# Kernel optimization log

Hardware: AMD Instinct MI355X
Metric: run time of the kernel (lower is better)

## Reference

```python
import jax, jax.numpy as jnp
import numpy as np


def setup_inputs() -> dict:
    key = jax.random.key(0)
    ks = jax.random.split(key, 5)
    B, C_in, C_out, H, W, k = 16, 64, 64, 256, 256, 16
    scale = 1.0 / (C_in * C_out)
    return {
        "u": jax.random.normal(ks[0], (B, C_in, H, W), dtype=jnp.float32),
        "W_pos_re": scale * jax.random.normal(ks[1], (C_in, C_out, k, k), dtype=jnp.float32),
        "W_pos_im": scale * jax.random.normal(ks[2], (C_in, C_out, k, k), dtype=jnp.float32),
        "W_neg_re": scale * jax.random.normal(ks[3], (C_in, C_out, k, k), dtype=jnp.float32),
        "W_neg_im": scale * jax.random.normal(ks[4], (C_in, C_out, k, k), dtype=jnp.float32),
    }


def reference(u, W_pos_re, W_pos_im, W_neg_re, W_neg_im):
    B, C_in, H, W = u.shape
    C_out = W_pos_re.shape[1]
    k = W_pos_re.shape[2]
    W_half = W // 2 + 1
    k_h = min(k, H // 2)
    k_w = min(k, W_half)

    R_pos = (W_pos_re + 1j * W_pos_im)[:, :, :k_h, :k_w]  # (C_in, C_out, k_h, k_w)
    R_neg = (W_neg_re + 1j * W_neg_im)[:, :, :k_h, :k_w]

    u_hat = jnp.fft.rfft2(u, norm="ortho")  # (B, C_in, H, W_half) complex

    # spectral multiply on retained modes only
    top = jnp.einsum("bchw,cohw->bohw", u_hat[:, :, :k_h, :k_w], R_pos)
    bot = jnp.einsum("bchw,cohw->bohw", u_hat[:, :, H - k_h:, :k_w], R_neg)

    v_hat = jnp.zeros((B, C_out, H, W_half), dtype=u_hat.dtype)
    v_hat = v_hat.at[:, :, :k_h, :k_w].set(top)
    v_hat = v_hat.at[:, :, H - k_h:, :k_w].set(bot)

    return jnp.fft.irfft2(v_hat, s=(H, W), norm="ortho")  # (B, C_out, H, W) real
```

## Files before the change

kernel.cpp:

```cpp
#include <hip/hip_runtime.h>


#define B_    16
#define H_    256
#define W_    256

#define OFF_CT 0
#define OFF_ST 256
#define OFF_RP 512
#define RP_SZ  (512*4096*2)
#define OFF_U  (OFF_RP + RP_SZ)
#define U_SZ   (1024*512*2)
#define OFF_V  (OFF_U + U_SZ)

#define UTP   260
#define TWOPI_256 0.024543692606170259f

typedef const __attribute__((address_space(1))) void g_void;
typedef __attribute__((address_space(3))) void l_void;

__device__ __forceinline__ void load_lds16(const float* g, float* l) {
    __builtin_amdgcn_global_load_lds((g_void*)g, (l_void*)l, 16, 0, 0);
}

__global__ __launch_bounds__(256) void k_fwd1(const float* __restrict__ u,
                                              const float* __restrict__ wpr,
                                              const float* __restrict__ wpi,
                                              const float* __restrict__ wnr,
                                              const float* __restrict__ wni,
                                              float* __restrict__ ws,
                                              float* __restrict__ P) {
    __shared__ __align__(16) float ut[32][UTP];
    int t = threadIdx.x;

    if (blockIdx.x >= 8192) {
        int mw = blockIdx.x - 8192;
        int m = mw >> 4, wmc = mw & 15;
        const float* wr; const float* wi; int i;
        if (m < 16) { wr = wpr; wi = wpi; i = m; }
        else        { wr = wnr; wi = wni; i = m - 16; }
        if (mw == 0) {
            double a = 2.0 * 3.14159265358979323846 * (double)t / 256.0;
            ws[OFF_CT + t] = (float)cos(a);
            ws[OFF_ST + t] = (float)sin(a);
        }
        float norm = (wmc == 0 ? 1.f : 2.f) * (1.f / 65536.f);
        int off = i * 16 + wmc;
        float2* rp = (float2*)(ws + OFF_RP) + (size_t)mw * 4096;
        #pragma unroll
        for (int k = 0; k < 16; ++k) {
            int co = t + 256 * k;
            rp[co] = make_float2(wr[(size_t)co * 256 + off] * norm,
                                 wi[(size_t)co * 256 + off] * norm);
        }
        return;
    }

    int bc = blockIdx.x >> 3, ch = blockIdx.x & 7;
    const float* ub = u + (size_t)bc * 65536 + ch * 8192;
    int lane = t & 63, w = t >> 6;
    #pragma unroll
    for (int k = 0; k < 8; ++k)
        load_lds16(ub + (w * 8 + k) * 256 + lane * 4, &ut[w * 8 + k][0]);

    int h = lane & 7, r8 = lane >> 3;
    int rowc = w * 8 + r8;
    int wm0 = 2 * h, wm1 = wm0 + 1;
    float s0v, c0v, s1v, c1v;
    __sincosf(TWOPI_256 * (float)wm0, &s0v, &c0v);
    __sincosf(TWOPI_256 * (float)wm1, &s1v, &c1v);
    float r0r = c0v, r0i = -s0v;
    float r1r = c1v, r1i = -s1v;
    float bs  = (h & 1) ? -1.f : 1.f;
    float dsg = (h & 1) ? 1.f : -1.f;

    float p0r = 0.f, p0i = 0.f, p1r = 0.f, p1i = 0.f;
    float t0r = 1.f, t0i = 0.f, t1r = 1.f, t1i = 0.f;

    asm volatile("s_waitcnt vmcnt(0)" ::: "memory");

    const float* rowp = &ut[rowc][0];
    #pragma unroll 4
    for (int bat = 0; bat < 16; ++bat) {
        const float* rp = rowp + 4 * bat;
        float4 q0 = *(const float4*)(rp);
        float4 q1 = *(const float4*)(rp + 64);
        float4 q2 = *(const float4*)(rp + 128);
        float4 q3 = *(const float4*)(rp + 192);
        #define PROC_(u0, u1, u2, u3) {                                   \
            float a_ = (u0) + (u2), b_ = (u1) + (u3);                     \
            float c_ = (u0) - (u2), d_ = (u1) - (u3);                     \
            float g0 = fmaf(bs, b_, a_);                                  \
            float g1r = c_, g1i = dsg * d_;                               \
            p0r = fmaf(g0, t0r, p0r);                                     \
            p0i = fmaf(g0, t0i, p0i);                                     \
            p1r = fmaf(g1r, t1r, fmaf(-g1i, t1i, p1r));                   \
            p1i = fmaf(g1r, t1i, fmaf( g1i, t1r, p1i));                   \
            float n0r = t0r * r0r - t0i * r0i;                            \
            float n0i = t0r * r0i + t0i * r0r;                            \
            float n1r = t1r * r1r - t1i * r1i;                            \
            float n1i = t1r * r1i + t1i * r1r;                            \
            t0r = n0r; t0i = n0i; t1r = n1r; t1i = n1i; }
        PROC_(q0.x, q1.x, q2.x, q3.x)
        PROC_(q0.y, q1.y, q2.y, q3.y)
        PROC_(q0.z, q1.z, q2.z, q3.z)
        PROC_(q0.w, q1.w, q2.w, q3.w)
        #undef PROC_
    }
    int y = ch * 32 + rowc;
    ((float4*)P)[((size_t)bc * 256 + y) * 8 + h] = make_float4(p0r, p0i, p1r, p1i);
}

__global__ __launch_bounds__(256) void k_fwd2(const float* __restrict__ P,
                                              float* __restrict__ ws) {
    __shared__ float Pl[256][36];
    int t = threadIdx.x, bc = blockIdx.x;
    const float4* Pg = (const float4*)(P + (size_t)bc * 8192);
    #pragma unroll
    for (int k = 0; k < 8; ++k) {
        int f4 = t + 256 * k;
        int y = f4 >> 3, q = f4 & 7;
        *(float4*)&Pl[y][q * 4] = Pg[f4];
    }
    __syncthreads();

    int wm = t & 15;
    int v  = t >> 4;
    int m1 = ((v & 3) << 2) | (v >> 2);
    float sv, cv;
    __sincosf(TWOPI_256 * (float)m1, &sv, &cv);
    float r1r = cv, r1i = -sv;
    __sincosf(TWOPI_256 * (float)(m1 - 16), &sv, &cv);
    float r2r = cv, r2i = -sv;
    float t1r = 1.f, t1i = 0.f, t2r = 1.f, t2i = 0.f;
    float U1r = 0.f, U1i = 0.f, U2r = 0.f, U2i = 0.f;
    int md = m1 & 3;
    #pragma unroll 4
    for (int yy = 0; yy < 64; ++yy) {
        float2 P0 = *(float2*)&Pl[yy][2 * wm];
        float2 P1 = *(float2*)&Pl[yy + 64][2 * wm];
        float2 P2 = *(float2*)&Pl[yy + 128][2 * wm];
        float2 P3 = *(float2*)&Pl[yy + 192][2 * wm];
        float ar = P0.x + P2.x, ai = P0.y + P2.y;
        float br = P1.x + P3.x, bi = P1.y + P3.y;
        float cr = P0.x - P2.x, ci = P0.y - P2.y;
        float dr = P1.x - P3.x, di = P1.y - P3.y;
        float gr, gi;
        if (md == 0)      { gr = ar + br; gi = ai + bi; }
        else if (md == 1) { gr = cr + di; gi = ci - dr; }
        else if (md == 2) { gr = ar - br; gi = ai - bi; }
        else              { gr = cr - di; gi = ci + dr; }
        U1r = fmaf(gr, t1r, fmaf(-gi, t1i, U1r));
        U1i = fmaf(gr, t1i, fmaf( gi, t1r, U1i));
        U2r = fmaf(gr, t2r, fmaf(-gi, t2i, U2r));
        U2i = fmaf(gr, t2i, fmaf( gi, t2r, U2i));
        float n1r = t1r * r1r - t1i * r1i, n1i = t1r * r1i + t1i * r1r;
        float n2r = t2r * r2r - t2i * r2i, n2i = t2r * r2i + t2i * r2r;
        t1r = n1r; t1i = n1i; t2r = n2r; t2i = n2i;
    }
    float2* U = (float2*)(ws + OFF_U) + (size_t)bc * 512;
    U[m1 * 16 + wm]          = make_float2(U1r, U1i);
    U[(m1 + 16) * 16 + wm]   = make_float2(U2r, U2i);
}

__global__ __launch_bounds__(256) void k_cgemm(float* __restrict__ ws) {
    __shared__ float2 Ul[1024];
    int mw = blockIdx.x, t = threadIdx.x;
    const float2* Ug = (const float2*)(ws + OFF_U);
    #pragma unroll
    for (int k = 0; k < 4; ++k) {
        int bcv = t + 256 * k;
        Ul[bcv] = Ug[(size_t)bcv * 512 + mw];
    }
    __syncthreads();
    int o = t & 63, bq = t >> 6;
    const float2* rp = (const float2*)(ws + OFF_RP) + (size_t)mw * 4096;
    float ar[4] = {0.f, 0.f, 0.f, 0.f}, ai[4] = {0.f, 0.f, 0.f, 0.f};
    #pragma unroll 4
    for (int c = 0; c < 64; ++c) {
        float2 R = rp[c * 64 + o];
        #pragma unroll
        for (int j = 0; j < 4; ++j) {
            float2 Uv = Ul[(bq * 4 + j) * 64 + c];
            ar[j] = fmaf(Uv.x, R.x, fmaf(-Uv.y, R.y, ar[j]));
            ai[j] = fmaf(Uv.x, R.y, fmaf( Uv.y, R.x, ai[j]));
        }
    }
    float2* Vg = (float2*)(ws + OFF_V) + (size_t)mw * 1024;
    #pragma unroll
    for (int j = 0; j < 4; ++j)
        Vg[(bq * 4 + j) * 64 + o] = make_float2(ar[j], ai[j]);
}

__global__ __launch_bounds__(256) void k_inv(const float* __restrict__ ws,
                                             float* __restrict__ out) {
    __shared__ float Vl[16][68];
    __shared__ float Tl[4][16][36];
    __shared__ float ct[256], st[256];
    int t = threadIdx.x;
    int bo = blockIdx.x >> 2, q = blockIdx.x & 3;
    ct[t] = ws[OFF_CT + t];
    st[t] = ws[OFF_ST + t];
    {
        const float2* Vg = (const float2*)(ws + OFF_V);
        float2 v0 = Vg[(size_t)t * 1024 + bo];
        float2 v1 = Vg[(size_t)(t + 256) * 1024 + bo];
        int m = t >> 4, wmv = t & 15;
        Vl[wmv][2 * m]        = v0.x;  Vl[wmv][2 * m + 1]        = v0.y;
        Vl[wmv][2 * (m + 16)] = v1.x;  Vl[wmv][2 * (m + 16) + 1] = v1.y;
    }
    __syncthreads();

    int wm4 = t & 15, yb = t >> 4;
    int y0 = q * 16 + yb;
    float vr[32], vi[32];
    #pragma unroll
    for (int m = 0; m < 32; ++m) { vr[m] = Vl[wm4][2 * m]; vi[m] = Vl[wm4][2 * m + 1]; }
    float cy = ct[y0], sy = st[y0];
    float T0r=0,T0i=0,T1r=0,T1i=0,T2r=0,T2i=0,T3r=0,T3i=0;
    float tr = 1.f, ti = 0.f;
    #pragma unroll
    for (int m = 0; m < 32; ++m) {
        if (m == 16) {
            int i16 = (4096 - 16 * y0) & 255;
            tr = ct[i16]; ti = st[i16];
        }
        float hr = vr[m] * tr - vi[m] * ti;
        float hi = vr[m] * ti + vi[m] * tr;
        const int md = m & 3;
        T0r += hr; T0i += hi;
        if (md == 0)      { T1r += hr; T1i += hi; T2r += hr; T2i += hi; T3r += hr; T3i += hi; }
        else if (md == 1) { T1r -= hi; T1i += hr; T2r -= hr; T2i -= hi; T3r += hi; T3i -= hr; }
        else if (md == 2) { T1r -= hr; T1i -= hi; T2r += hr; T2i += hi; T3r -= hr; T3i -= hi; }
        else              { T1r += hi; T1i -= hr; T2r -= hr; T2i -= hi; T3r -= hi; T3i += hr; }
        float nr = tr * cy - ti * sy, ni = tr * sy + ti * cy;
        tr = nr; ti = ni;
    }
    Tl[0][yb][wm4] = T0r; Tl[0][yb][16 + wm4] = T0i;
    Tl[1][yb][wm4] = T1r; Tl[1][yb][16 + wm4] = T1i;
    Tl[2][yb][wm4] = T2r; Tl[2][yb][16 + wm4] = T2i;
    Tl[3][yb][wm4] = T3r; Tl[3][yb][16 + wm4] = T3i;
    __syncthreads();

    int l = t & 63, wv = t >> 6;
    float c0[16], s0[16];
    #pragma unroll
    for (int wm = 0; wm < 16; ++wm) {
        int idx = (wm * l) & 255;
        c0[wm] = ct[idx]; s0[wm] = st[idx];
    }
    float* ob = out + (size_t)bo * 65536;
    for (int yi = 0; yi < 16; ++yi) {
        int y = wv * 64 + q * 16 + yi;
        float TR[16], TI[16];
        const float4* rowv = (const float4*)&Tl[wv][yi][0];
        #pragma unroll
        for (int qq = 0; qq < 4; ++qq) {
            float4 a = rowv[qq];
            TR[4*qq]=a.x; TR[4*qq+1]=a.y; TR[4*qq+2]=a.z; TR[4*qq+3]=a.w;
            float4 b = rowv[qq + 4];
            TI[4*qq]=b.x; TI[4*qq+1]=b.y; TI[4*qq+2]=b.z; TI[4*qq+3]=b.w;
        }
        float Pv = 0.f, Qv = 0.f, Rv = 0.f, Sv = 0.f;
        #pragma unroll
        for (int wm = 0; wm < 16; wm += 2) {
            Pv = fmaf(TR[wm],     c0[wm],     Pv);
            Rv = fmaf(TI[wm],     s0[wm],     Rv);
            Qv = fmaf(TR[wm + 1], c0[wm + 1], Qv);
            Sv = fmaf(TI[wm + 1], s0[wm + 1], Sv);
        }
        float Ac = Pv + Qv, Bs = Rv + Sv;
        float Dc = Pv - Qv, Es = Rv - Sv;
        float* row = ob + (size_t)y * 256;
        row[l]               = Ac - Bs;
        row[(256 - l) & 255] = Ac + Bs;
        row[128 + l]         = Dc - Es;
        row[128 - l]         = Dc + Es;
        float E0 = TR[0] + TR[4] + TR[8]  + TR[12];
        float E2 = TR[2] + TR[6] + TR[10] + TR[14];
        float O1 = TI[1] + TI[5] + TI[9]  + TI[13];
        float O3 = TI[3] + TI[7] + TI[11] + TI[15];
        float EC = E0 - E2, OC = O1 - O3;
        if (l == 0) {
            row[64]  = EC - OC;
            row[192] = EC + OC;
        }
    }
}

extern "C" void kernel_launch(void* const* d_in, const int* in_sizes, int n_in,
                              void* d_out, int out_size, void* d_ws, size_t ws_size,
                              hipStream_t stream) {
    const float* u   = (const float*)d_in[0];
    const float* wpr = (const float*)d_in[1];
    const float* wpi = (const float*)d_in[2];
    const float* wnr = (const float*)d_in[3];
    const float* wni = (const float*)d_in[4];
    float* out = (float*)d_out;
    float* ws  = (float*)d_ws;
    float* P   = (float*)d_out;

    hipLaunchKernelGGL(k_fwd1,  dim3(8704), dim3(256), 0, stream, u, wpr, wpi, wnr, wni, ws, P);
    hipLaunchKernelGGL(k_fwd2,  dim3(1024), dim3(256), 0, stream, P, ws);
    hipLaunchKernelGGL(k_cgemm, dim3(512),  dim3(256), 0, stream, ws);
    hipLaunchKernelGGL(k_inv,   dim3(4096), dim3(256), 0, stream, ws, out);
}
```

Baseline: 207.1 us.

## Read input directly in fwd1 and split fwd2 column DFT across two blocks

```diff
diff --git a/kernel.cpp b/kernel.cpp
--- a/kernel.cpp
+++ b/kernel.cpp
@@ -9,19 +9,13 @@
 #define OFF_ST 256
 #define OFF_RP 512
 #define RP_SZ  (512*4096*2)
-#define OFF_U  (OFF_RP + RP_SZ)
+#define OFF_U0 (OFF_RP + RP_SZ)
 #define U_SZ   (1024*512*2)
-#define OFF_V  (OFF_U + U_SZ)
-
-#define UTP   260
+#define OFF_V  (OFF_U0 + U_SZ)
+#define V_SZ   (512*1024*2)
+#define OFF_U1 (OFF_V + V_SZ)
+
 #define TWOPI_256 0.024543692606170259f
-
-typedef const __attribute__((address_space(1))) void g_void;
-typedef __attribute__((address_space(3))) void l_void;
-
-__device__ __forceinline__ void load_lds16(const float* g, float* l) {
-    __builtin_amdgcn_global_load_lds((g_void*)g, (l_void*)l, 16, 0, 0);
-}
 
 __global__ __launch_bounds__(256) void k_fwd1(const float* __restrict__ u,
                                               const float* __restrict__ wpr,
@@ -30,7 +24,6 @@
                                               const float* __restrict__ wni,
                                               float* __restrict__ ws,
                                               float* __restrict__ P) {
-    __shared__ __align__(16) float ut[32][UTP];
     int t = threadIdx.x;
 
     if (blockIdx.x >= 8192) {
@@ -57,14 +50,11 @@
     }
 
     int bc = blockIdx.x >> 3, ch = blockIdx.x & 7;
-    const float* ub = u + (size_t)bc * 65536 + ch * 8192;
     int lane = t & 63, w = t >> 6;
-    #pragma unroll
-    for (int k = 0; k < 8; ++k)
-        load_lds16(ub + (w * 8 + k) * 256 + lane * 4, &ut[w * 8 + k][0]);
-
     int h = lane & 7, r8 = lane >> 3;
     int rowc = w * 8 + r8;
+    const float* rowp = u + (size_t)bc * 65536 + ch * 8192 + rowc * 256;
+
     int wm0 = 2 * h, wm1 = wm0 + 1;
     float s0v, c0v, s1v, c1v;
     __sincosf(TWOPI_256 * (float)wm0, &s0v, &c0v);
@@ -77,16 +67,13 @@
     float p0r = 0.f, p0i = 0.f, p1r = 0.f, p1i = 0.f;
     float t0r = 1.f, t0i = 0.f, t1r = 1.f, t1i = 0.f;
 
-    asm volatile("s_waitcnt vmcnt(0)" ::: "memory");
-
-    const float* rowp = &ut[rowc][0];
     #pragma unroll 4
     for (int bat = 0; bat < 16; ++bat) {
-        const float* rp = rowp + 4 * bat;
-        float4 q0 = *(const float4*)(rp);
-        float4 q1 = *(const float4*)(rp + 64);
-        float4 q2 = *(const float4*)(rp + 128);
-        float4 q3 = *(const float4*)(rp + 192);
+        const float4* rp4 = (const float4*)(rowp + 4 * bat);
+        float4 q0 = rp4[0];
+        float4 q1 = rp4[16];
+        float4 q2 = rp4[32];
+        float4 q3 = rp4[48];
         #define PROC_(u0, u1, u2, u3) {                                   \
             float a_ = (u0) + (u2), b_ = (u1) + (u3);                     \
             float c_ = (u0) - (u2), d_ = (u1) - (u3);                     \
@@ -113,14 +100,15 @@
 
 __global__ __launch_bounds__(256) void k_fwd2(const float* __restrict__ P,
                                               float* __restrict__ ws) {
-    __shared__ float Pl[256][36];
-    int t = threadIdx.x, bc = blockIdx.x;
+    __shared__ float Pl[4][32][36];
+    int t = threadIdx.x;
+    int bc = blockIdx.x >> 1, hh = blockIdx.x & 1;
     const float4* Pg = (const float4*)(P + (size_t)bc * 8192);
     #pragma unroll
-    for (int k = 0; k < 8; ++k) {
-        int f4 = t + 256 * k;
-        int y = f4 >> 3, q = f4 & 7;
-        *(float4*)&Pl[y][q * 4] = Pg[f4];
+    for (int k = 0; k < 4; ++k) {
+        int idx = t + 256 * k;
+        int g = idx >> 8, j = (idx >> 3) & 31, q = idx & 7;
+        *(float4*)&Pl[g][j][4 * q] = Pg[(size_t)(hh * 32 + j + 64 * g) * 8 + q];
     }
     __syncthreads();
 
@@ -132,15 +120,17 @@
     float r1r = cv, r1i = -sv;
     __sincosf(TWOPI_256 * (float)(m1 - 16), &sv, &cv);
     float r2r = cv, r2i = -sv;
-    float t1r = 1.f, t1i = 0.f, t2r = 1.f, t2i = 0.f;
+    int a0 = (m1 * 32 * hh) & 255;
+    __sincosf(TWOPI_256 * (float)a0, &sv, &cv);
+    float t1r = cv, t1i = -sv, t2r = cv, t2i = -sv;
     float U1r = 0.f, U1i = 0.f, U2r = 0.f, U2i = 0.f;
     int md = m1 & 3;
     #pragma unroll 4
-    for (int yy = 0; yy < 64; ++yy) {
-        float2 P0 = *(float2*)&Pl[yy][2 * wm];
-        float2 P1 = *(float2*)&Pl[yy + 64][2 * wm];
-        float2 P2 = *(float2*)&Pl[yy + 128][2 * wm];
-        float2 P3 = *(float2*)&Pl[yy + 192][2 * wm];
+    for (int j = 0; j < 32; ++j) {
+        float2 P0 = *(float2*)&Pl[0][j][2 * wm];
+        float2 P1 = *(float2*)&Pl[1][j][2 * wm];
+        float2 P2 = *(float2*)&Pl[2][j][2 * wm];
+        float2 P3 = *(float2*)&Pl[3][j][2 * wm];
         float ar = P0.x + P2.x, ai = P0.y + P2.y;
         float br = P1.x + P3.x, bi = P1.y + P3.y;
         float cr = P0.x - P2.x, ci = P0.y - P2.y;
@@ -158,19 +148,22 @@
         float n2r = t2r * r2r - t2i * r2i, n2i = t2r * r2i + t2i * r2r;
         t1r = n1r; t1i = n1i; t2r = n2r; t2i = n2i;
     }
-    float2* U = (float2*)(ws + OFF_U) + (size_t)bc * 512;
-    U[m1 * 16 + wm]          = make_float2(U1r, U1i);
-    U[(m1 + 16) * 16 + wm]   = make_float2(U2r, U2i);
+    float2* U = (float2*)(ws + (hh ? OFF_U1 : OFF_U0)) + (size_t)bc * 512;
+    U[m1 * 16 + wm]        = make_float2(U1r, U1i);
+    U[(m1 + 16) * 16 + wm] = make_float2(U2r, U2i);
 }
 
 __global__ __launch_bounds__(256) void k_cgemm(float* __restrict__ ws) {
     __shared__ float2 Ul[1024];
     int mw = blockIdx.x, t = threadIdx.x;
-    const float2* Ug = (const float2*)(ws + OFF_U);
+    const float2* Ug0 = (const float2*)(ws + OFF_U0);
+    const float2* Ug1 = (const float2*)(ws + OFF_U1);
     #pragma unroll
     for (int k = 0; k < 4; ++k) {
         int bcv = t + 256 * k;
-        Ul[bcv] = Ug[(size_t)bcv * 512 + mw];
+        float2 a = Ug0[(size_t)bcv * 512 + mw];
+        float2 b = Ug1[(size_t)bcv * 512 + mw];
+        Ul[bcv] = make_float2(a.x + b.x, a.y + b.y);
     }
     __syncthreads();
     int o = t & 63, bq = t >> 6;
@@ -301,7 +294,7 @@
     float* P   = (float*)d_out;
 
     hipLaunchKernelGGL(k_fwd1,  dim3(8704), dim3(256), 0, stream, u, wpr, wpi, wnr, wni, ws, P);
-    hipLaunchKernelGGL(k_fwd2,  dim3(1024), dim3(256), 0, stream, P, ws);
+    hipLaunchKernelGGL(k_fwd2,  dim3(2048), dim3(256), 0, stream, P, ws);
     hipLaunchKernelGGL(k_cgemm, dim3(512),  dim3(256), 0, stream, ws);
     hipLaunchKernelGGL(k_inv,   dim3(4096), dim3(256), 0, stream, ws, out);
 }
```

After: 233.1 us. 1.13x slower.

## Split row DFT across lane quads and reduce partial sums with DPP

Applied to the files above, without the earlier changes.

```diff
diff --git a/kernel.cpp b/kernel.cpp
--- a/kernel.cpp
+++ b/kernel.cpp
@@ -1,9 +1,5 @@
 #include <hip/hip_runtime.h>
 
-
-#define B_    16
-#define H_    256
-#define W_    256
 
 #define OFF_CT 0
 #define OFF_ST 256
@@ -21,6 +17,12 @@
 
 __device__ __forceinline__ void load_lds16(const float* g, float* l) {
     __builtin_amdgcn_global_load_lds((g_void*)g, (l_void*)l, 16, 0, 0);
+}
+
+template<int CTRL>
+__device__ __forceinline__ float dppf(float x) {
+    return __int_as_float(__builtin_amdgcn_update_dpp(
+        0, __float_as_int(x), CTRL, 0xF, 0xF, true));
 }
 
 __global__ __launch_bounds__(256) void k_fwd1(const float* __restrict__ u,
@@ -63,52 +65,85 @@
     for (int k = 0; k < 8; ++k)
         load_lds16(ub + (w * 8 + k) * 256 + lane * 4, &ut[w * 8 + k][0]);
 
-    int h = lane & 7, r8 = lane >> 3;
+    int s = lane & 3, h = (lane >> 2) & 1, r8 = lane >> 3;
     int rowc = w * 8 + r8;
-    int wm0 = 2 * h, wm1 = wm0 + 1;
-    float s0v, c0v, s1v, c1v;
-    __sincosf(TWOPI_256 * (float)wm0, &s0v, &c0v);
-    __sincosf(TWOPI_256 * (float)wm1, &s1v, &c1v);
-    float r0r = c0v, r0i = -s0v;
-    float r1r = c1v, r1i = -s1v;
-    float bs  = (h & 1) ? -1.f : 1.f;
-    float dsg = (h & 1) ? 1.f : -1.f;
-
-    float p0r = 0.f, p0i = 0.f, p1r = 0.f, p1i = 0.f;
-    float t0r = 1.f, t0i = 0.f, t1r = 1.f, t1i = 0.f;
+
+    float sv, cv;
+    __sincosf(TWOPI_256 * 1.f, &sv, &cv);
+    float rb1r = cv, rb1i = -sv;
+    __sincosf(TWOPI_256 * (float)(8 * h), &sv, &cv);
+    float r8hr = cv, r8hi = -sv;
+    int j0 = 16 * s;
+    __sincosf(TWOPI_256 * (float)((8 * h * j0) & 255), &sv, &cv);
+    float tw0r = cv, tw0i = -sv;
+    __sincosf(TWOPI_256 * (float)j0, &sv, &cv);
+    float bjr = cv, bji = -sv;
+
+    float a0r=0,a0i=0,a1r=0,a1i=0,a2r=0,a2i=0,a3r=0,a3i=0;
+    float a4r=0,a4i=0,a5r=0,a5i=0,a6r=0,a6i=0,a7r=0,a7i=0;
 
     asm volatile("s_waitcnt vmcnt(0)" ::: "memory");
 
-    const float* rowp = &ut[rowc][0];
-    #pragma unroll 4
-    for (int bat = 0; bat < 16; ++bat) {
-        const float* rp = rowp + 4 * bat;
-        float4 q0 = *(const float4*)(rp);
-        float4 q1 = *(const float4*)(rp + 64);
-        float4 q2 = *(const float4*)(rp + 128);
-        float4 q3 = *(const float4*)(rp + 192);
-        #define PROC_(u0, u1, u2, u3) {                                   \
-            float a_ = (u0) + (u2), b_ = (u1) + (u3);                     \
-            float c_ = (u0) - (u2), d_ = (u1) - (u3);                     \
-            float g0 = fmaf(bs, b_, a_);                                  \
-            float g1r = c_, g1i = dsg * d_;                               \
-            p0r = fmaf(g0, t0r, p0r);                                     \
-            p0i = fmaf(g0, t0i, p0i);                                     \
-            p1r = fmaf(g1r, t1r, fmaf(-g1i, t1i, p1r));                   \
-            p1i = fmaf(g1r, t1i, fmaf( g1i, t1r, p1i));                   \
-            float n0r = t0r * r0r - t0i * r0i;                            \
-            float n0i = t0r * r0i + t0i * r0r;                            \
-            float n1r = t1r * r1r - t1i * r1i;                            \
-            float n1i = t1r * r1i + t1i * r1r;                            \
-            t0r = n0r; t0i = n0i; t1r = n1r; t1i = n1i; }
-        PROC_(q0.x, q1.x, q2.x, q3.x)
-        PROC_(q0.y, q1.y, q2.y, q3.y)
-        PROC_(q0.z, q1.z, q2.z, q3.z)
-        PROC_(q0.w, q1.w, q2.w, q3.w)
-        #undef PROC_
-    }
-    int y = ch * 32 + rowc;
-    ((float4*)P)[((size_t)bc * 256 + y) * 8 + h] = make_float4(p0r, p0i, p1r, p1i);
+    const float* q0p = &ut[rowc][j0];
+    #define CMUL_(tr_, ti_) { float nr_ = tr_*bjr - ti_*bji,                \
+          ni_ = tr_*bji + ti_*bjr; tr_ = nr_; ti_ = ni_; }
+    #define STEP_(u0,u1,u2,u3) {                                            \
+        float Av_=(u0)+(u2), Bv_=(u1)+(u3), Cv_=(u0)-(u2), Dv_=(u1)-(u3);   \
+        float gp_ = Av_ + Bv_, gm_ = Av_ - Bv_;                             \
+        float twr = tw0r, twi = tw0i;                                       \
+        a0r = fmaf(gp_, twr, a0r); a0i = fmaf(gp_, twi, a0i);               \
+        CMUL_(twr, twi)                                                     \
+        a1r = fmaf(Cv_, twr, fmaf( Dv_, twi, a1r));                         \
+        a1i = fmaf(Cv_, twi, fmaf(-Dv_, twr, a1i));                         \
+        CMUL_(twr, twi)                                                     \
+        a2r = fmaf(gm_, twr, a2r); a2i = fmaf(gm_, twi, a2i);               \
+        CMUL_(twr, twi)                                                     \
+        a3r = fmaf(Cv_, twr, fmaf(-Dv_, twi, a3r));                         \
+        a3i = fmaf(Cv_, twi, fmaf( Dv_, twr, a3i));                         \
+        CMUL_(twr, twi)                                                     \
+        a4r = fmaf(gp_, twr, a4r); a4i = fmaf(gp_, twi, a4i);               \
+        CMUL_(twr, twi)                                                     \
+        a5r = fmaf(Cv_, twr, fmaf( Dv_, twi, a5r));                         \
+        a5i = fmaf(Cv_, twi, fmaf(-Dv_, twr, a5i));                         \
+        CMUL_(twr, twi)                                                     \
+        a6r = fmaf(gm_, twr, a6r); a6i = fmaf(gm_, twi, a6i);               \
+        CMUL_(twr, twi)                                                     \
+        a7r = fmaf(Cv_, twr, fmaf(-Dv_, twi, a7r));                         \
+        a7i = fmaf(Cv_, twi, fmaf( Dv_, twr, a7i));                         \
+        { float nr = tw0r*r8hr - tw0i*r8hi, ni = tw0r*r8hi + tw0i*r8hr;     \
+          tw0r = nr; tw0i = ni; }                                           \
+        { float nr = bjr*rb1r - bji*rb1i, ni = bjr*rb1i + bji*rb1r;         \
+          bjr = nr; bji = ni; } }
+
+    #pragma unroll
+    for (int g = 0; g < 4; ++g) {
+        float4 x0 = *(const float4*)(q0p + 4 * g);
+        float4 x1 = *(const float4*)(q0p + 64  + 4 * g);
+        float4 x2 = *(const float4*)(q0p + 128 + 4 * g);
+        float4 x3 = *(const float4*)(q0p + 192 + 4 * g);
+        STEP_(x0.x, x1.x, x2.x, x3.x)
+        STEP_(x0.y, x1.y, x2.y, x3.y)
+        STEP_(x0.z, x1.z, x2.z, x3.z)
+        STEP_(x0.w, x1.w, x2.w, x3.w)
+    }
+    #undef STEP_
+    #undef CMUL_
+
+    #define RED_(v) { v += dppf<0xB1>(v); v += dppf<0x4E>(v); }
+    RED_(a0r) RED_(a0i) RED_(a1r) RED_(a1i)
+    RED_(a2r) RED_(a2i) RED_(a3r) RED_(a3i)
+    RED_(a4r) RED_(a4i) RED_(a5r) RED_(a5i)
+    RED_(a6r) RED_(a6i) RED_(a7r) RED_(a7i)
+    #undef RED_
+
+    if ((lane & 3) == 0) {
+        int y = ch * 32 + rowc;
+        float4* Pp = (float4*)P + (((size_t)bc * 256 + y) * 8 + 4 * h);
+        Pp[0] = make_float4(a0r, a0i, a1r, a1i);
+        Pp[1] = make_float4(a2r, a2i, a3r, a3i);
+        Pp[2] = make_float4(a4r, a4i, a5r, a5i);
+        Pp[3] = make_float4(a6r, a6i, a7r, a7i);
+    }
 }
 
 __global__ __launch_bounds__(256) void k_fwd2(const float* __restrict__ P,
```

Measured after the change: 204.7 us (median of 2 runs). Within noise of the previous version (-1.2%).
